# Performance work log

Measured on AMD Instinct MI355X. Metric: run time of the kernel, lower is better.

The kernel has to match this reference:

```python
import jax, jax.numpy as jnp
import numpy as np

VOCAB = 32000
ROUTE_BIAS = 10.0  # weight on the deterministic one-hot route vs mu logits


def setup_inputs() -> dict:
    key = jax.random.key(0)
    k1, k2, k3, k4, k5, k6 = jax.random.split(key, 6)
    B, S, H = 2, 4096, 1024
    E, Ie = 8, 512  # intermediate_size=4096 -> expert_intermediate=512, fused dim=2*Ie=1024
    return {
        "hidden_states": jax.random.normal(k1, (B, S, H), dtype=jnp.float32),
        "token_ids": jax.random.randint(k2, (B, S), 0, VOCAB),
        "mu": jax.random.normal(k3, (B, S, H), dtype=jnp.float32),
        "gate_up_proj": jax.random.normal(k4, (E, H, 2 * Ie), dtype=jnp.float32) * 0.02,
        "down_proj": jax.random.normal(k5, (E, Ie, H), dtype=jnp.float32) * 0.02,
        "mu_router_w": jax.random.normal(k6, (E, H), dtype=jnp.float32) * 0.02,
    }


def reference(hidden_states, token_ids, mu, gate_up_proj, down_proj, mu_router_w):
    B, S, H = hidden_states.shape
    E, _, F2 = gate_up_proj.shape
    Ie = F2 // 2
    N = B * S

    # deterministic token->expert routing, optionally perturbed by mu logits
    token_to_expert = jnp.arange(VOCAB, dtype=jnp.int32) % E
    base_expert = token_to_expert[jnp.clip(token_ids, 0, VOCAB - 1)]      # [B,S]
    mu_logits = jnp.einsum('bsh,eh->bse', mu, mu_router_w)                 # [B,S,E]
    combined = jax.nn.one_hot(base_expert, E, dtype=mu_logits.dtype) * ROUTE_BIAS + mu_logits
    expert_ids = jnp.argmax(combined, axis=-1).reshape(N)                  # [N]

    x = hidden_states.reshape(N, H)
    tok = jnp.arange(N)

    # compute per-expert GEMM then select per-token expert output
    # (same math as gathering the full weight slab per token, without the
    #  N*H*2Ie gathered-weight blowup of the original torch code)
    gu_all = jnp.einsum('nh,ehf->enf', x, gate_up_proj)                    # [E,N,2Ie]
    gu = gu_all[expert_ids, tok]                                           # [N,2Ie]
    gate, up = gu[:, :Ie], gu[:, Ie:]
    inter = jax.nn.silu(gate) * up                                         # [N,Ie]

    z_all = jnp.einsum('ni,eih->enh', inter, down_proj)                    # [E,N,H]
    out = z_all[expert_ids, tok].reshape(B, S, H)
    return out
```

## Files before the change

kernel.cpp:

```cpp
#include <hip/hip_runtime.h>
#include <hip/hip_bf16.h>
#include <stdint.h>

typedef __bf16 bf16x8 __attribute__((ext_vector_type(8)));
typedef float f32x4 __attribute__((ext_vector_type(4)));

#define ROUTE_BIAS_F 10.0f
#define VOCAB_SZ 32000

__device__ __forceinline__ unsigned short f2bf(float f) {
    union { float f; unsigned u; } v; v.f = f;
    unsigned u = v.u;
    unsigned r = u + 0x7FFFu + ((u >> 16) & 1u);
    return (unsigned short)(r >> 16);
}
__device__ __forceinline__ float bf2f(unsigned short s) {
    union { unsigned u; float f; } v; v.u = ((unsigned)s) << 16;
    return v.f;
}

__global__ void k_convert_bf16(const float* __restrict__ in,
                               unsigned short* __restrict__ out, int n) {
    int i = (blockIdx.x * blockDim.x + threadIdx.x) * 4;
    if (i + 3 < n) {
        float4 f = *(const float4*)(in + i);
        ushort4 o;
        o.x = f2bf(f.x); o.y = f2bf(f.y); o.z = f2bf(f.z); o.w = f2bf(f.w);
        *(ushort4*)(out + i) = o;
    } else {
        for (; i < n; ++i) out[i] = f2bf(in[i]);
    }
}

__global__ void k_transpose_bf16(const float* __restrict__ in,
                                 unsigned short* __restrict__ out, int R, int C) {
    __shared__ float tile[32][33];
    int e = blockIdx.z;
    const float* inp = in + (size_t)e * R * C;
    unsigned short* outp = out + (size_t)e * R * C;
    int c0 = blockIdx.x * 32, r0 = blockIdx.y * 32;
    int tx = threadIdx.x, ty = threadIdx.y;
#pragma unroll
    for (int k = 0; k < 32; k += 8)
        tile[ty + k][tx] = inp[(size_t)(r0 + ty + k) * C + c0 + tx];
    __syncthreads();
#pragma unroll
    for (int k = 0; k < 32; k += 8)
        outp[(size_t)(c0 + ty + k) * R + r0 + tx] = f2bf(tile[tx][ty + k]);
}

__global__ void k_logits(const float* __restrict__ mu, const int* __restrict__ tok_ids,
                         const float* __restrict__ rw, int H, int N,
                         int* __restrict__ eids) {
    int lane = threadIdx.x & 63;
    int wv   = threadIdx.x >> 6;
    int tok  = blockIdx.x * 4 + wv;
    if (tok >= N) return;
    float acc[8];
#pragma unroll
    for (int e = 0; e < 8; ++e) acc[e] = 0.f;
    const float* m = mu + (size_t)tok * H;
    for (int h = lane; h < H; h += 64) {
        float mv = m[h];
#pragma unroll
        for (int e = 0; e < 8; ++e) acc[e] += mv * rw[e * H + h];
    }
#pragma unroll
    for (int e = 0; e < 8; ++e) {
        float v = acc[e];
#pragma unroll
        for (int off = 32; off > 0; off >>= 1) v += __shfl_xor(v, off);
        acc[e] = v;
    }
    if (lane == 0) {
        int t = tok_ids[tok];
        if (t < 0) t = 0;
        if (t > VOCAB_SZ - 1) t = VOCAB_SZ - 1;
        int be = t % 8;
        float best = -1e30f; int bi = 0;
#pragma unroll
        for (int e = 0; e < 8; ++e) {
            float v = acc[e] + (e == be ? ROUTE_BIAS_F : 0.f);
            if (v > best) { best = v; bi = e; }
        }
        eids[tok] = bi;
    }
}

__global__ void k_count(const int* __restrict__ eids,
                        int* __restrict__ blockcnt, int N) {
    __shared__ int cnt[8];
    int tid = threadIdx.x;
    if (tid < 8) cnt[tid] = 0;
    __syncthreads();
    int tok = blockIdx.x * 256 + tid;
    int lane = tid & 63;
    int eid = (tok < N) ? eids[tok] : -1;
#pragma unroll
    for (int e = 0; e < 8; ++e) {
        unsigned long long m = __ballot(eid == e);
        if (lane == 0 && m) atomicAdd(&cnt[e], __popcll(m));
    }
    __syncthreads();
    if (tid < 8) blockcnt[blockIdx.x * 8 + tid] = cnt[tid];
}

__global__ void k_scan(const int* __restrict__ blockcnt,
                       int* __restrict__ counts, int* __restrict__ base_,
                       int* __restrict__ offs, int NB) {
    __shared__ int scnt[8];
    int e = threadIdx.x;
    if (e < 8) {
        int s = 0;
        for (int b = 0; b < NB; ++b) {
            offs[b * 8 + e] = s;
            s += blockcnt[b * 8 + e];
        }
        scnt[e] = s;
        counts[e] = s;
    }
    __syncthreads();
    if (e == 0) {
        int s = 0;
#pragma unroll
        for (int i = 0; i < 8; ++i) { base_[i] = s; s += scnt[i]; }
    }
}

__global__ void k_scatter(const int* __restrict__ eids,
                          const int* __restrict__ offs,
                          int* __restrict__ list, int N) {
    __shared__ int wavecnt[4][8];
    int tid = threadIdx.x;
    int lane = tid & 63, wv = tid >> 6;
    int tok = blockIdx.x * 256 + tid;
    int eid = (tok < N) ? eids[tok] : -1;
    unsigned long long below = (1ull << lane) - 1ull;
    int myrank = 0;
#pragma unroll
    for (int e = 0; e < 8; ++e) {
        unsigned long long m = __ballot(eid == e);
        if (lane == 0) wavecnt[wv][e] = __popcll(m);
        if (eid == e) myrank = __popcll(m & below);
    }
    __syncthreads();
    if (eid >= 0) {
        int pre = 0;
        for (int w = 0; w < wv; ++w) pre += wavecnt[w][eid];
        int pos = offs[blockIdx.x * 8 + eid] + pre + myrank;
        list[eid * N + pos] = tok;
    }
}

#define TM 128
#define TN 128
#define TK 64
#define LDSP 72

__global__ __launch_bounds__(256, 2) void k_gemm_gateup(
    const unsigned short* __restrict__ X,
    const unsigned short* __restrict__ Wt,
    unsigned short* __restrict__ GU,
    const int* __restrict__ counts, const int* __restrict__ base_,
    const int* __restrict__ list, int N, int H, int F2) {
    int e = blockIdx.z, mt = blockIdx.y, nt = blockIdx.x;
    int cnt = counts[e];
    int m0 = mt * TM;
    if (m0 >= cnt) return;
    int n0 = nt * TN;

    __shared__ __align__(16) unsigned short As[TM * LDSP];
    __shared__ __align__(16) unsigned short Bs[TN * LDSP];

    int tid = threadIdx.x;
    int lane = tid & 63, wid = tid >> 6;
    int wm = (wid >> 1) * 64, wn = (wid & 1) * 64;

    f32x4 acc[4][4];
#pragma unroll
    for (int i = 0; i < 4; ++i)
#pragma unroll
        for (int j = 0; j < 4; ++j) acc[i][j] = (f32x4)(0.f);

    const unsigned short* We = Wt + ((size_t)e * F2 + n0) * H;

    const unsigned short* aptr[4];
#pragma unroll
    for (int i = 0; i < 4; ++i) {
        int chunk = tid + 256 * i;
        int r = chunk >> 3;
        int gr = m0 + r;
        aptr[i] = (gr < cnt) ? X + (size_t)list[e * N + gr] * H : nullptr;
    }

    for (int k0 = 0; k0 < H; k0 += TK) {
#pragma unroll
        for (int i = 0; i < 4; ++i) {
            int chunk = tid + 256 * i;
            int r = chunk >> 3, cc = (chunk & 7) * 8;
            uint4 v = make_uint4(0u, 0u, 0u, 0u);
            if (aptr[i]) v = *(const uint4*)(aptr[i] + k0 + cc);
            *(uint4*)&As[r * LDSP + cc] = v;
        }
#pragma unroll
        for (int i = 0; i < 4; ++i) {
            int chunk = tid + 256 * i;
            int r = chunk >> 3, cc = (chunk & 7) * 8;
            uint4 v = *(const uint4*)(We + (size_t)r * H + k0 + cc);
            *(uint4*)&Bs[r * LDSP + cc] = v;
        }
        __syncthreads();
#pragma unroll
        for (int ks = 0; ks < TK; ks += 32) {
            bf16x8 af[4], bfr[4];
            int kk = ks + (lane >> 4) * 8;
            int rA = wm + (lane & 15);
            int rB = wn + (lane & 15);
#pragma unroll
            for (int im = 0; im < 4; ++im)
                af[im] = *(const bf16x8*)&As[(rA + im * 16) * LDSP + kk];
#pragma unroll
            for (int in_ = 0; in_ < 4; ++in_)
                bfr[in_] = *(const bf16x8*)&Bs[(rB + in_ * 16) * LDSP + kk];
#pragma unroll
            for (int im = 0; im < 4; ++im)
#pragma unroll
                for (int in_ = 0; in_ < 4; ++in_)
                    acc[im][in_] = __builtin_amdgcn_mfma_f32_16x16x32_bf16(
                        af[im], bfr[in_], acc[im][in_], 0, 0, 0);
        }
        __syncthreads();
    }

    int b = base_[e];
#pragma unroll
    for (int im = 0; im < 4; ++im) {
#pragma unroll
        for (int j = 0; j < 4; ++j) {
            int row = wm + im * 16 + (lane >> 4) * 4 + j;
            int gr = m0 + row;
            if (gr < cnt) {
                unsigned short* orow = GU + (size_t)(b + gr) * F2 + n0;
#pragma unroll
                for (int in_ = 0; in_ < 4; ++in_) {
                    int col = wn + in_ * 16 + (lane & 15);
                    orow[col] = f2bf(acc[im][in_][j]);
                }
            }
        }
    }
}

__global__ void k_silu(const unsigned short* __restrict__ GU,
                       unsigned short* __restrict__ IT, int N, int Ie) {
    int idx = blockIdx.x * blockDim.x + threadIdx.x;
    if (idx >= N * Ie) return;
    int r = idx / Ie, c = idx - r * Ie;
    float g = bf2f(GU[(size_t)r * 2 * Ie + c]);
    float u = bf2f(GU[(size_t)r * 2 * Ie + Ie + c]);
    float s = g / (1.f + __expf(-g));
    IT[idx] = f2bf(s * u);
}

__global__ __launch_bounds__(256, 2) void k_gemm_down(
    const unsigned short* __restrict__ IT,
    const unsigned short* __restrict__ Wt,
    float* __restrict__ OUT,
    const int* __restrict__ counts, const int* __restrict__ base_,
    const int* __restrict__ list, int N, int Ie, int H) {
    int e = blockIdx.z, mt = blockIdx.y, nt = blockIdx.x;
    int cnt = counts[e];
    int m0 = mt * TM;
    if (m0 >= cnt) return;
    int n0 = nt * TN;
    int b = base_[e];

    __shared__ __align__(16) unsigned short As[TM * LDSP];
    __shared__ __align__(16) unsigned short Bs[TN * LDSP];

    int tid = threadIdx.x;
    int lane = tid & 63, wid = tid >> 6;
    int wm = (wid >> 1) * 64, wn = (wid & 1) * 64;

    f32x4 acc[4][4];
#pragma unroll
    for (int i = 0; i < 4; ++i)
#pragma unroll
        for (int j = 0; j < 4; ++j) acc[i][j] = (f32x4)(0.f);

    const unsigned short* We = Wt + ((size_t)e * H + n0) * Ie;

    const unsigned short* aptr[4];
#pragma unroll
    for (int i = 0; i < 4; ++i) {
        int chunk = tid + 256 * i;
        int r = chunk >> 3;
        int gr = m0 + r;
        aptr[i] = (gr < cnt) ? IT + (size_t)(b + gr) * Ie : nullptr;
    }

    for (int k0 = 0; k0 < Ie; k0 += TK) {
#pragma unroll
        for (int i = 0; i < 4; ++i) {
            int chunk = tid + 256 * i;
            int r = chunk >> 3, cc = (chunk & 7) * 8;
            uint4 v = make_uint4(0u, 0u, 0u, 0u);
            if (aptr[i]) v = *(const uint4*)(aptr[i] + k0 + cc);
            *(uint4*)&As[r * LDSP + cc] = v;
        }
#pragma unroll
        for (int i = 0; i < 4; ++i) {
            int chunk = tid + 256 * i;
            int r = chunk >> 3, cc = (chunk & 7) * 8;
            uint4 v = *(const uint4*)(We + (size_t)r * Ie + k0 + cc);
            *(uint4*)&Bs[r * LDSP + cc] = v;
        }
        __syncthreads();
#pragma unroll
        for (int ks = 0; ks < TK; ks += 32) {
            bf16x8 af[4], bfr[4];
            int kk = ks + (lane >> 4) * 8;
            int rA = wm + (lane & 15);
            int rB = wn + (lane & 15);
#pragma unroll
            for (int im = 0; im < 4; ++im)
                af[im] = *(const bf16x8*)&As[(rA + im * 16) * LDSP + kk];
#pragma unroll
            for (int in_ = 0; in_ < 4; ++in_)
                bfr[in_] = *(const bf16x8*)&Bs[(rB + in_ * 16) * LDSP + kk];
#pragma unroll
            for (int im = 0; im < 4; ++im)
#pragma unroll
                for (int in_ = 0; in_ < 4; ++in_)
                    acc[im][in_] = __builtin_amdgcn_mfma_f32_16x16x32_bf16(
                        af[im], bfr[in_], acc[im][in_], 0, 0, 0);
        }
        __syncthreads();
    }

#pragma unroll
    for (int im = 0; im < 4; ++im) {
#pragma unroll
        for (int j = 0; j < 4; ++j) {
            int row = wm + im * 16 + (lane >> 4) * 4 + j;
            int gr = m0 + row;
            if (gr < cnt) {
                int tok = list[e * N + gr];
                float* orow = OUT + (size_t)tok * H + n0;
#pragma unroll
                for (int in_ = 0; in_ < 4; ++in_) {
                    int col = wn + in_ * 16 + (lane & 15);
                    orow[col] = acc[im][in_][j];
                }
            }
        }
    }
}

extern "C" void kernel_launch(void* const* d_in, const int* in_sizes, int n_in,
                              void* d_out, int out_size, void* d_ws, size_t ws_size,
                              hipStream_t stream) {
    const float* hidden   = (const float*)d_in[0];
    const int*   tok_ids  = (const int*)d_in[1];
    const float* mu       = (const float*)d_in[2];
    const float* gup      = (const float*)d_in[3];
    const float* dnp      = (const float*)d_in[4];
    const float* rw       = (const float*)d_in[5];
    float* out = (float*)d_out;

    int N  = in_sizes[1];
    int H  = in_sizes[0] / N;
    int E  = in_sizes[5] / H;
    int F2 = in_sizes[3] / (E * H);
    int Ie = F2 / 2;

    int NB = (N + 255) / 256;

    char* ws = (char*)d_ws;
    size_t o = 0;
    auto alloc = [&](size_t sz) {
        size_t r = o;
        o += (sz + 255) & ~(size_t)255;
        return r;
    };
    int* counts   = (int*)(ws + alloc((size_t)E * 4));
    int* base_    = (int*)(ws + alloc((size_t)E * 4));
    int* eids     = (int*)(ws + alloc((size_t)N * 4));
    int* blockcnt = (int*)(ws + alloc((size_t)NB * 8 * 4));
    int* offs     = (int*)(ws + alloc((size_t)NB * 8 * 4));
    int* list     = (int*)(ws + alloc((size_t)E * N * 4));
    unsigned short* xb   = (unsigned short*)(ws + alloc((size_t)N * H * 2));
    unsigned short* wgut = (unsigned short*)(ws + alloc((size_t)E * F2 * H * 2));
    unsigned short* wdnt = (unsigned short*)(ws + alloc((size_t)E * H * Ie * 2));
    unsigned short* gu   = (unsigned short*)(ws + alloc((size_t)N * F2 * 2));
    unsigned short* inter = xb;

    k_convert_bf16<<<dim3((N * H / 4 + 255) / 256), dim3(256), 0, stream>>>(hidden, xb, N * H);

    dim3 tb(32, 8);
    k_transpose_bf16<<<dim3(F2 / 32, H / 32, E), tb, 0, stream>>>(gup, wgut, H, F2);
    k_transpose_bf16<<<dim3(H / 32, Ie / 32, E), tb, 0, stream>>>(dnp, wdnt, Ie, H);

    k_logits<<<dim3((N + 3) / 4), dim3(256), 0, stream>>>(mu, tok_ids, rw, H, N, eids);
    k_count<<<dim3(NB), dim3(256), 0, stream>>>(eids, blockcnt, N);
    k_scan<<<dim3(1), dim3(64), 0, stream>>>(blockcnt, counts, base_, offs, NB);
    k_scatter<<<dim3(NB), dim3(256), 0, stream>>>(eids, offs, list, N);

    dim3 g1(F2 / TN, (N + TM - 1) / TM, E);
    k_gemm_gateup<<<g1, dim3(256), 0, stream>>>(xb, wgut, gu, counts, base_, list, N, H, F2);

    k_silu<<<dim3((N * Ie + 255) / 256), dim3(256), 0, stream>>>(gu, inter, N, Ie);

    dim3 g2(H / TN, (N + TM - 1) / TM, E);
    k_gemm_down<<<g2, dim3(256), 0, stream>>>(inter, wdnt, out, counts, base_, list, N, Ie, H);
}
```

Measured before the change: 266.6 us.

## Use direct global-to-LDS loads with XOR swizzle, vectorize SiLU, parallelize scan

Both expert GEMMs now load A and B tiles with global_load_lds 16-byte transfers straight into an unpadded LDS layout. An XOR swizzle on the 16-byte chunk index stands in for the old padding to avoid bank conflicts. The SiLU kernel handles 8 elements per thread with vector loads and stores, and the expert-count scan is turned into a 64-lane shuffle scan. Rows past the expert count now read a valid dummy row instead of being zero-filled, which relies on the output store masking those rows out.

```diff
diff --git a/kernel.cpp b/kernel.cpp
--- a/kernel.cpp
+++ b/kernel.cpp
@@ -17,6 +17,11 @@
 __device__ __forceinline__ float bf2f(unsigned short s) {
     union { unsigned u; float f; } v; v.u = ((unsigned)s) << 16;
     return v.f;
+}
+__device__ __forceinline__ void ld16(const unsigned short* g, unsigned short* l) {
+    __builtin_amdgcn_global_load_lds(
+        (const __attribute__((address_space(1))) void*)g,
+        (__attribute__((address_space(3))) void*)l, 16, 0, 0);
 }
 
 __global__ void k_convert_bf16(const float* __restrict__ in,
@@ -108,22 +113,28 @@
 __global__ void k_scan(const int* __restrict__ blockcnt,
                        int* __restrict__ counts, int* __restrict__ base_,
                        int* __restrict__ offs, int NB) {
-    __shared__ int scnt[8];
-    int e = threadIdx.x;
-    if (e < 8) {
-        int s = 0;
-        for (int b = 0; b < NB; ++b) {
-            offs[b * 8 + e] = s;
-            s += blockcnt[b * 8 + e];
-        }
-        scnt[e] = s;
-        counts[e] = s;
-    }
+    __shared__ int tot[8];
+    int lane = threadIdx.x;
+    int e = lane >> 3, g = lane & 7;
+    int v[4];
+    int s = 0;
+#pragma unroll
+    for (int i = 0; i < 4; ++i) { v[i] = s; s += blockcnt[(g * 4 + i) * 8 + e]; }
+    int inc = s;
+#pragma unroll
+    for (int d = 1; d < 8; d <<= 1) {
+        int t = __shfl_up(inc, d);
+        if (g >= d) inc += t;
+    }
+    int excl = inc - s;
+#pragma unroll
+    for (int i = 0; i < 4; ++i) offs[(g * 4 + i) * 8 + e] = excl + v[i];
+    if (g == 7) { counts[e] = inc; tot[e] = inc; }
     __syncthreads();
-    if (e == 0) {
-        int s = 0;
-#pragma unroll
-        for (int i = 0; i < 8; ++i) { base_[i] = s; s += scnt[i]; }
+    if (lane == 0) {
+        int s2 = 0;
+#pragma unroll
+        for (int i = 0; i < 8; ++i) { base_[i] = s2; s2 += tot[i]; }
     }
 }
 
@@ -155,7 +166,6 @@
 #define TM 128
 #define TN 128
 #define TK 64
-#define LDSP 72
 
 __global__ __launch_bounds__(256, 2) void k_gemm_gateup(
     const unsigned short* __restrict__ X,
@@ -169,12 +179,27 @@
     if (m0 >= cnt) return;
     int n0 = nt * TN;
 
-    __shared__ __align__(16) unsigned short As[TM * LDSP];
-    __shared__ __align__(16) unsigned short Bs[TN * LDSP];
+    __shared__ __align__(16) unsigned short As[TM * TK];
+    __shared__ __align__(16) unsigned short Bs[TN * TK];
 
     int tid = threadIdx.x;
-    int lane = tid & 63, wid = tid >> 6;
-    int wm = (wid >> 1) * 64, wn = (wid & 1) * 64;
+    int lane = tid & 63, wv = tid >> 6;
+    int wm = (wv >> 1) * 64, wn = (wv & 1) * 64;
+
+    int rowg = lane >> 3;
+    int sl   = (lane & 7) ^ rowg;
+
+    const unsigned short* We = Wt + ((size_t)e * F2 + n0) * H;
+    const unsigned short* ag[4];
+    const unsigned short* bg[4];
+#pragma unroll
+    for (int i = 0; i < 4; ++i) {
+        int r = wv * 32 + i * 8 + rowg;
+        int gr = m0 + r;
+        int tokrow = (gr < cnt) ? list[e * N + gr] : 0;
+        ag[i] = X + (size_t)tokrow * H + sl * 8;
+        bg[i] = We + (size_t)r * H + sl * 8;
+    }
 
     f32x4 acc[4][4];
 #pragma unroll
@@ -182,46 +207,28 @@
 #pragma unroll
         for (int j = 0; j < 4; ++j) acc[i][j] = (f32x4)(0.f);
 
-    const unsigned short* We = Wt + ((size_t)e * F2 + n0) * H;
-
-    const unsigned short* aptr[4];
-#pragma unroll
-    for (int i = 0; i < 4; ++i) {
-        int chunk = tid + 256 * i;
-        int r = chunk >> 3;
-        int gr = m0 + r;
-        aptr[i] = (gr < cnt) ? X + (size_t)list[e * N + gr] * H : nullptr;
-    }
+    int q = lane >> 4, m = lane & 15;
+    int sw = m & 7;
 
     for (int k0 = 0; k0 < H; k0 += TK) {
 #pragma unroll
-        for (int i = 0; i < 4; ++i) {
-            int chunk = tid + 256 * i;
-            int r = chunk >> 3, cc = (chunk & 7) * 8;
-            uint4 v = make_uint4(0u, 0u, 0u, 0u);
-            if (aptr[i]) v = *(const uint4*)(aptr[i] + k0 + cc);
-            *(uint4*)&As[r * LDSP + cc] = v;
-        }
-#pragma unroll
-        for (int i = 0; i < 4; ++i) {
-            int chunk = tid + 256 * i;
-            int r = chunk >> 3, cc = (chunk & 7) * 8;
-            uint4 v = *(const uint4*)(We + (size_t)r * H + k0 + cc);
-            *(uint4*)&Bs[r * LDSP + cc] = v;
-        }
+        for (int i = 0; i < 4; ++i)
+            ld16(ag[i] + k0, &As[(wv * 32 + i * 8) * TK]);
+#pragma unroll
+        for (int i = 0; i < 4; ++i)
+            ld16(bg[i] + k0, &Bs[(wv * 32 + i * 8) * TK]);
         __syncthreads();
 #pragma unroll
         for (int ks = 0; ks < TK; ks += 32) {
+            int kc = ks >> 3;
+            int ck = ((kc + q) ^ sw) << 3;
             bf16x8 af[4], bfr[4];
-            int kk = ks + (lane >> 4) * 8;
-            int rA = wm + (lane & 15);
-            int rB = wn + (lane & 15);
 #pragma unroll
             for (int im = 0; im < 4; ++im)
-                af[im] = *(const bf16x8*)&As[(rA + im * 16) * LDSP + kk];
+                af[im] = *(const bf16x8*)&As[(wm + m + im * 16) * TK + ck];
 #pragma unroll
             for (int in_ = 0; in_ < 4; ++in_)
-                bfr[in_] = *(const bf16x8*)&Bs[(rB + in_ * 16) * LDSP + kk];
+                bfr[in_] = *(const bf16x8*)&Bs[(wn + m + in_ * 16) * TK + ck];
 #pragma unroll
             for (int im = 0; im < 4; ++im)
 #pragma unroll
@@ -254,12 +261,27 @@
 __global__ void k_silu(const unsigned short* __restrict__ GU,
                        unsigned short* __restrict__ IT, int N, int Ie) {
     int idx = blockIdx.x * blockDim.x + threadIdx.x;
-    if (idx >= N * Ie) return;
-    int r = idx / Ie, c = idx - r * Ie;
-    float g = bf2f(GU[(size_t)r * 2 * Ie + c]);
-    float u = bf2f(GU[(size_t)r * 2 * Ie + Ie + c]);
-    float s = g / (1.f + __expf(-g));
-    IT[idx] = f2bf(s * u);
+    int total = (N * Ie) >> 3;
+    if (idx >= total) return;
+    int per_row = Ie >> 3;
+    int r = idx / per_row, c = (idx - r * per_row) * 8;
+    const unsigned short* g8 = GU + (size_t)r * 2 * Ie + c;
+    const unsigned short* u8 = g8 + Ie;
+    ushort4 ga = *(const ushort4*)g8, gb = *(const ushort4*)(g8 + 4);
+    ushort4 ua = *(const ushort4*)u8, ub = *(const ushort4*)(u8 + 4);
+    unsigned short o[8];
+    unsigned short gs[8] = {ga.x, ga.y, ga.z, ga.w, gb.x, gb.y, gb.z, gb.w};
+    unsigned short us[8] = {ua.x, ua.y, ua.z, ua.w, ub.x, ub.y, ub.z, ub.w};
+#pragma unroll
+    for (int i = 0; i < 8; ++i) {
+        float g = bf2f(gs[i]), u = bf2f(us[i]);
+        float s = g / (1.f + __expf(-g));
+        o[i] = f2bf(s * u);
+    }
+    ushort4 oa = {o[0], o[1], o[2], o[3]}, ob = {o[4], o[5], o[6], o[7]};
+    unsigned short* op = IT + (size_t)r * Ie + c;
+    *(ushort4*)op = oa;
+    *(ushort4*)(op + 4) = ob;
 }
 
 __global__ __launch_bounds__(256, 2) void k_gemm_down(
@@ -275,12 +297,27 @@
     int n0 = nt * TN;
     int b = base_[e];
 
-    __shared__ __align__(16) unsigned short As[TM * LDSP];
-    __shared__ __align__(16) unsigned short Bs[TN * LDSP];
+    __shared__ __align__(16) unsigned short As[TM * TK];
+    __shared__ __align__(16) unsigned short Bs[TN * TK];
 
     int tid = threadIdx.x;
-    int lane = tid & 63, wid = tid >> 6;
-    int wm = (wid >> 1) * 64, wn = (wid & 1) * 64;
+    int lane = tid & 63, wv = tid >> 6;
+    int wm = (wv >> 1) * 64, wn = (wv & 1) * 64;
+
+    int rowg = lane >> 3;
+    int sl   = (lane & 7) ^ rowg;
+
+    const unsigned short* We = Wt + ((size_t)e * H + n0) * Ie;
+    const unsigned short* ag[4];
+    const unsigned short* bg[4];
+#pragma unroll
+    for (int i = 0; i < 4; ++i) {
+        int r = wv * 32 + i * 8 + rowg;
+        int gr = m0 + r;
+        int arow = (gr < cnt) ? (b + gr) : b;
+        ag[i] = IT + (size_t)arow * Ie + sl * 8;
+        bg[i] = We + (size_t)r * Ie + sl * 8;
+    }
 
     f32x4 acc[4][4];
 #pragma unroll
@@ -288,46 +325,28 @@
 #pragma unroll
         for (int j = 0; j < 4; ++j) acc[i][j] = (f32x4)(0.f);
 
-    const unsigned short* We = Wt + ((size_t)e * H + n0) * Ie;
-
-    const unsigned short* aptr[4];
-#pragma unroll
-    for (int i = 0; i < 4; ++i) {
-        int chunk = tid + 256 * i;
-        int r = chunk >> 3;
-        int gr = m0 + r;
-        aptr[i] = (gr < cnt) ? IT + (size_t)(b + gr) * Ie : nullptr;
-    }
+    int q = lane >> 4, m = lane & 15;
+    int sw = m & 7;
 
     for (int k0 = 0; k0 < Ie; k0 += TK) {
 #pragma unroll
-        for (int i = 0; i < 4; ++i) {
-            int chunk = tid + 256 * i;
-            int r = chunk >> 3, cc = (chunk & 7) * 8;
-            uint4 v = make_uint4(0u, 0u, 0u, 0u);
-            if (aptr[i]) v = *(const uint4*)(aptr[i] + k0 + cc);
-            *(uint4*)&As[r * LDSP + cc] = v;
-        }
-#pragma unroll
-        for (int i = 0; i < 4; ++i) {
-            int chunk = tid + 256 * i;
-            int r = chunk >> 3, cc = (chunk & 7) * 8;
-            uint4 v = *(const uint4*)(We + (size_t)r * Ie + k0 + cc);
-            *(uint4*)&Bs[r * LDSP + cc] = v;
-        }
+        for (int i = 0; i < 4; ++i)
+            ld16(ag[i] + k0, &As[(wv * 32 + i * 8) * TK]);
+#pragma unroll
+        for (int i = 0; i < 4; ++i)
+            ld16(bg[i] + k0, &Bs[(wv * 32 + i * 8) * TK]);
         __syncthreads();
 #pragma unroll
         for (int ks = 0; ks < TK; ks += 32) {
+            int kc = ks >> 3;
+            int ck = ((kc + q) ^ sw) << 3;
             bf16x8 af[4], bfr[4];
-            int kk = ks + (lane >> 4) * 8;
-            int rA = wm + (lane & 15);
-            int rB = wn + (lane & 15);
 #pragma unroll
             for (int im = 0; im < 4; ++im)
-                af[im] = *(const bf16x8*)&As[(rA + im * 16) * LDSP + kk];
+                af[im] = *(const bf16x8*)&As[(wm + m + im * 16) * TK + ck];
 #pragma unroll
             for (int in_ = 0; in_ < 4; ++in_)
-                bfr[in_] = *(const bf16x8*)&Bs[(rB + in_ * 16) * LDSP + kk];
+                bfr[in_] = *(const bf16x8*)&Bs[(wn + m + in_ * 16) * TK + ck];
 #pragma unroll
             for (int im = 0; im < 4; ++im)
 #pragma unroll
@@ -409,7 +428,7 @@
     dim3 g1(F2 / TN, (N + TM - 1) / TM, E);
     k_gemm_gateup<<<g1, dim3(256), 0, stream>>>(xb, wgut, gu, counts, base_, list, N, H, F2);
 
-    k_silu<<<dim3((N * Ie + 255) / 256), dim3(256), 0, stream>>>(gu, inter, N, Ie);
+    k_silu<<<dim3((N * Ie / 8 + 255) / 256), dim3(256), 0, stream>>>(gu, inter, N, Ie);
 
     dim3 g2(H / TN, (N + TM - 1) / TM, E);
     k_gemm_down<<<g2, dim3(256), 0, stream>>>(inter, wdnt, out, counts, base_, list, N, Ie, H);
```

After: 245.1 us. 8.1% less time.
